# Kernel optimization log

Hardware: AMD Instinct MI355X
Metric: run time of the kernel (lower is better)

## Reference

```python
import jax, jax.numpy as jnp
import numpy as np

NUM_CATEGORIES = 32
INPUT_DIM = 1536
HIDDEN_DIM = 1024
OUTPUT_DIM = 1024
B, T = 128, 32


def setup_inputs() -> dict:
    key = jax.random.key(0)
    k_x, k_cat, k_w1, k_w2 = jax.random.split(key, 4)
    x = jax.random.normal(k_x, (B, T, INPUT_DIM), dtype=jnp.float32)
    cat_ids = jax.random.randint(k_cat, (B,), 0, NUM_CATEGORIES)
    # CategorySpecificLinear params: W ~ 0.02*randn, b = zeros
    W1 = 0.02 * jax.random.normal(k_w1, (NUM_CATEGORIES, INPUT_DIM, HIDDEN_DIM), dtype=jnp.float32)
    b1 = jnp.zeros((NUM_CATEGORIES, HIDDEN_DIM), dtype=jnp.float32)
    W2 = 0.02 * jax.random.normal(k_w2, (NUM_CATEGORIES, HIDDEN_DIM, OUTPUT_DIM), dtype=jnp.float32)
    b2 = jnp.zeros((NUM_CATEGORIES, OUTPUT_DIM), dtype=jnp.float32)
    return {"x": x, "cat_ids": cat_ids, "W1": W1, "b1": b1, "W2": W2, "b2": b2}


def _cat_linear(x, W, b, cat_ids):
    # x: (B, T, D_in); W: (C, D_in, D_out); b: (C, D_out)
    # torch: bmm(x, W[cat_ids]) + b[cat_ids].unsqueeze(1)
    return jnp.einsum("btd,bdh->bth", x, W[cat_ids]) + b[cat_ids][:, None, :]


def reference(x, cat_ids, W1, b1, W2, b2):
    # CategorySpecificMLP.forward
    hidden = jax.nn.relu(_cat_linear(x, W1, b1, cat_ids))  # (B, T, H)
    return _cat_linear(hidden, W2, b2, cat_ids)            # (B, T, O)
```

## Files before the change

kernel.cpp:

```cpp
#include <hip/hip_runtime.h>
#include <hip/hip_bf16.h>
#include <stdint.h>

#define NCAT 32
#define DIN  1536
#define DMID 1024
#define NB   128
#define TT   32

#define BM 128
#define BN 64
#define BK 32
#define LDA 40
#define MAXG 56

typedef __attribute__((ext_vector_type(8))) short short8;
typedef __attribute__((ext_vector_type(4))) float f32x4;

static __device__ __forceinline__ unsigned int pk2bf(float lo, float hi) {
  unsigned short a = __builtin_bit_cast(unsigned short, __float2bfloat16(lo));
  unsigned short b = __builtin_bit_cast(unsigned short, __float2bfloat16(hi));
  return ((unsigned int)b << 16) | (unsigned int)a;
}

static __device__ __forceinline__ void bar_noflush() {
  asm volatile("s_waitcnt lgkmcnt(0)" ::: "memory");
  __builtin_amdgcn_s_barrier();
  asm volatile("" ::: "memory");
}

__global__ void build_groups(const int* __restrict__ cat_ids, int* __restrict__ wsi) {
  __shared__ int cats[NB];
  __shared__ int cnt[NCAT];
  __shared__ int off[NCAT];
  int t = threadIdx.x;
  cats[t] = cat_ids[t];
  __syncthreads();
  if (t < NCAT) {
    int n = 0;
    for (int b = 0; b < NB; b++) n += (cats[b] == t);
    cnt[t] = n;
  }
  __syncthreads();
  if (t == 0) {
    int acc = 0;
    for (int c = 0; c < NCAT; c++) { off[c] = acc; acc += cnt[c]; }
  }
  __syncthreads();
  if (t < NCAT) {
    int o = off[t];
    for (int b = 0; b < NB; b++)
      if (cats[b] == t) wsi[o++] = b;
  }
  if (t == 0) {
    for (int s = 0; s < MAXG; s++) {
      wsi[132 + s * 4 + 0] = 0;
      wsi[132 + s * 4 + 1] = 0;
      wsi[132 + s * 4 + 2] = 0;
    }
    int rload[8];
    for (int r = 0; r < 8; r++) rload[r] = 0;
    for (int c = 0; c < NCAT; c++) {
      int n = cnt[c];
      if (n == 0) continue;
      int o = off[c];
      int r = 0;
      for (int k = 1; k < 8; k++) if (rload[k] < rload[r]) r = k;
      for (int j = 0; j < n; j += 4) {
        if (rload[r] >= 7) {
          r = 0;
          for (int k = 1; k < 8; k++) if (rload[k] < rload[r]) r = k;
        }
        int s = r + 8 * rload[r];
        rload[r]++;
        wsi[132 + s * 4 + 0] = c;
        wsi[132 + s * 4 + 1] = o + j;
        wsi[132 + s * 4 + 2] = (n - j) < 4 ? (n - j) : 4;
      }
    }
    wsi[128] = MAXG;
  }
}

template <int LAYER>
__global__ __launch_bounds__(256)
void mlp_gemm(const void* __restrict__ Ain, const float* __restrict__ W,
              const float* __restrict__ bias, const int* __restrict__ wsi,
              void* __restrict__ Out, int K) {
  const int l    = blockIdx.y * 16 + blockIdx.x;
  const int xcd  = l & 7;
  const int m    = l >> 3;
  const int slot = xcd + 8 * (m >> 4);
  const int cat   = wsi[132 + slot * 4 + 0];
  const int start = wsi[132 + slot * 4 + 1];
  const int cnt   = wsi[132 + slot * 4 + 2];
  if (cnt == 0) return;
  const int n0 = (m & 15) * BN;

  __shared__ unsigned short As[2][BM * LDA];
  __shared__ unsigned short Bs[2][4 * BN * 8];

  const int tid  = threadIdx.x;
  const int lane = tid & 63;
  const int w    = tid >> 6;

  const int arow  = tid >> 1;
  const int khalf = (tid & 1) * 16;
  const int lb    = arow >> 5;
  const int tok   = arow & 31;
  const int lbc   = lb < (cnt - 1) ? lb : (cnt - 1);
  const int batch = wsi[start + lbc];
  const long grow = (long)(batch * TT + tok);

  const float* Wcol = W + (size_t)cat * (size_t)K * 1024 + n0 + lane;

  f32x4 acc[4][2];
#pragma unroll
  for (int i = 0; i < 4; i++)
#pragma unroll
    for (int j = 0; j < 2; j++) acc[i][j] = (f32x4){0.f, 0.f, 0.f, 0.f};

  const int wm  = (w >> 1) * 64;
  const int wn  = (w & 1) * 32;
  const int kg  = lane >> 4;
  const int c16 = lane & 15;

  auto load_tile = [&](int k0, float4 ar[4], uint4 ah[2], float br[8]) {
    if constexpr (LAYER == 1) {
      const float* ap = (const float*)Ain + grow * (long)K + k0 + khalf;
      ar[0] = *(const float4*)(ap + 0);
      ar[1] = *(const float4*)(ap + 4);
      ar[2] = *(const float4*)(ap + 8);
      ar[3] = *(const float4*)(ap + 12);
    } else {
      const uint4* ap = (const uint4*)((const unsigned short*)Ain + grow * (long)K + k0 + khalf);
      ah[0] = ap[0];
      ah[1] = ap[1];
    }
    const float* bp = Wcol + (size_t)(k0 + w * 8) * 1024;
#pragma unroll
    for (int r = 0; r < 8; r++) br[r] = bp[(size_t)r * 1024];
  };

  auto store_tile = [&](int buf, const float4 ar[4], const uint4 ah[2], const float br[8]) {
    if constexpr (LAYER == 1) {
      uint4 aw0 = make_uint4(pk2bf(ar[0].x, ar[0].y), pk2bf(ar[0].z, ar[0].w),
                             pk2bf(ar[1].x, ar[1].y), pk2bf(ar[1].z, ar[1].w));
      uint4 aw1 = make_uint4(pk2bf(ar[2].x, ar[2].y), pk2bf(ar[2].z, ar[2].w),
                             pk2bf(ar[3].x, ar[3].y), pk2bf(ar[3].z, ar[3].w));
      *(uint4*)&As[buf][arow * LDA + khalf]     = aw0;
      *(uint4*)&As[buf][arow * LDA + khalf + 8] = aw1;
    } else {
      *(uint4*)&As[buf][arow * LDA + khalf]     = ah[0];
      *(uint4*)&As[buf][arow * LDA + khalf + 8] = ah[1];
    }
    uint4 bw = make_uint4(pk2bf(br[0], br[1]), pk2bf(br[2], br[3]),
                          pk2bf(br[4], br[5]), pk2bf(br[6], br[7]));
    *(uint4*)&Bs[buf][(w * BN + lane) * 8] = bw;
  };

  auto compute = [&](int buf) {
    short8 afrag[4], bfrag[2];
#pragma unroll
    for (int i = 0; i < 4; i++)
      afrag[i] = *(const short8*)&As[buf][(wm + i * 16 + c16) * LDA + kg * 8];
#pragma unroll
    for (int j = 0; j < 2; j++)
      bfrag[j] = *(const short8*)&Bs[buf][(kg * BN + wn + j * 16 + c16) * 8];
#pragma unroll
    for (int i = 0; i < 4; i++)
#pragma unroll
      for (int j = 0; j < 2; j++)
        acc[i][j] = __builtin_amdgcn_mfma_f32_16x16x32_bf16(afrag[i], bfrag[j], acc[i][j], 0, 0, 0);
  };

  float4 arA[4]; uint4 ahA[2]; float brA[8];
  float4 arB[4]; uint4 ahB[2]; float brB[8];

  const int nt = K / BK;

  load_tile(0, arA, ahA, brA);
  load_tile(BK, arB, ahB, brB);
  store_tile(0, arA, ahA, brA);
  bar_noflush();

  for (int t = 0; t + 2 <= nt; t += 2) {
    if (t + 2 < nt) load_tile((t + 2) * BK, arA, ahA, brA);
    store_tile(1, arB, ahB, brB);
    compute(0);
    bar_noflush();

    if (t + 3 < nt) load_tile((t + 3) * BK, arB, ahB, brB);
    if (t + 2 < nt) store_tile(0, arA, ahA, brA);
    compute(1);
    bar_noflush();
  }

  const int rquad = (lane >> 4) * 4;
#pragma unroll
  for (int i = 0; i < 4; i++) {
#pragma unroll
    for (int j = 0; j < 2; j++) {
      int gcol = n0 + wn + j * 16 + c16;
      float bb = bias[cat * 1024 + gcol];
#pragma unroll
      for (int r = 0; r < 4; r++) {
        int lrow = wm + i * 16 + rquad + r;
        int lb2 = lrow >> 5;
        if (lb2 < cnt) {
          int b2 = wsi[start + lb2];
          long orow = (long)(b2 * TT + (lrow & 31));
          float v = acc[i][j][r] + bb;
          if constexpr (LAYER == 1) {
            v = fmaxf(v, 0.f);
            ((unsigned short*)Out)[orow * DMID + gcol] =
                __builtin_bit_cast(unsigned short, __float2bfloat16(v));
          } else {
            ((float*)Out)[orow * 1024 + gcol] = v;
          }
        }
      }
    }
  }
}

extern "C" void kernel_launch(void* const* d_in, const int* in_sizes, int n_in,
                              void* d_out, int out_size, void* d_ws, size_t ws_size,
                              hipStream_t stream) {
  const float* x       = (const float*)d_in[0];
  const int*   cat_ids = (const int*)d_in[1];
  const float* W1      = (const float*)d_in[2];
  const float* b1      = (const float*)d_in[3];
  const float* W2      = (const float*)d_in[4];
  const float* b2      = (const float*)d_in[5];
  float* out = (float*)d_out;

  int* wsi = (int*)d_ws;
  unsigned short* hidden = (unsigned short*)((char*)d_ws + 8192);

  build_groups<<<dim3(1), dim3(128), 0, stream>>>(cat_ids, wsi);
  mlp_gemm<1><<<dim3(1024 / BN, MAXG), dim3(256), 0, stream>>>(
      (const void*)x, W1, b1, wsi, (void*)hidden, DIN);
  mlp_gemm<2><<<dim3(1024 / BN, MAXG), dim3(256), 0, stream>>>(
      (const void*)hidden, W2, b2, wsi, (void*)out, DMID);
}
```

Baseline: 486.3 us.

## Stream A tiles into LDS via direct global-to-LDS loads with swizzled layout

```diff
diff --git a/kernel.cpp b/kernel.cpp
--- a/kernel.cpp
+++ b/kernel.cpp
@@ -11,7 +11,6 @@
 #define BM 128
 #define BN 64
 #define BK 32
-#define LDA 40
 #define MAXG 56
 
 typedef __attribute__((ext_vector_type(8))) short short8;
@@ -23,10 +22,15 @@
   return ((unsigned int)b << 16) | (unsigned int)a;
 }
 
-static __device__ __forceinline__ void bar_noflush() {
-  asm volatile("s_waitcnt lgkmcnt(0)" ::: "memory");
-  __builtin_amdgcn_s_barrier();
-  asm volatile("" ::: "memory");
+static __device__ __forceinline__ unsigned int cvtpk(float lo, float hi) {
+  unsigned int r;
+  asm volatile("v_cvt_pk_bf16_f32 %0, %1, %2" : "=v"(r) : "v"(lo), "v"(hi));
+  return r;
+}
+
+static __device__ __forceinline__ void dma16(const void* g, void* l) {
+  __builtin_amdgcn_global_load_lds((const __attribute__((address_space(1))) void*)g,
+                                   (__attribute__((address_space(3))) void*)l, 16, 0, 0);
 }
 
 __global__ void build_groups(const int* __restrict__ cat_ids, int* __restrict__ wsi) {
@@ -97,73 +101,86 @@
   if (cnt == 0) return;
   const int n0 = (m & 15) * BN;
 
-  __shared__ unsigned short As[2][BM * LDA];
+  constexpr int ROWB   = (LAYER == 1) ? 128 : 64;
+  constexpr int ABYTES = BM * ROWB;
+  __shared__ __align__(16) unsigned char Asmem[2][ABYTES];
   __shared__ unsigned short Bs[2][4 * BN * 8];
 
   const int tid  = threadIdx.x;
   const int lane = tid & 63;
   const int w    = tid >> 6;
 
-  const int arow  = tid >> 1;
-  const int khalf = (tid & 1) * 16;
-  const int lb    = arow >> 5;
-  const int tok   = arow & 31;
-  const int lbc   = lb < (cnt - 1) ? lb : (cnt - 1);
-  const int batch = wsi[start + lbc];
-  const long grow = (long)(batch * TT + tok);
-
-  const float* Wcol = W + (size_t)cat * (size_t)K * 1024 + n0 + lane;
-
-  f32x4 acc[4][2];
-#pragma unroll
-  for (int i = 0; i < 4; i++)
-#pragma unroll
-    for (int j = 0; j < 2; j++) acc[i][j] = (f32x4){0.f, 0.f, 0.f, 0.f};
-
   const int wm  = (w >> 1) * 64;
   const int wn  = (w & 1) * 32;
   const int kg  = lane >> 4;
+  const int kg2 = kg << 1;
   const int c16 = lane & 15;
 
-  auto load_tile = [&](int k0, float4 ar[4], uint4 ah[2], float br[8]) {
+  const int batchW = wsi[start + (w < cnt ? w : cnt - 1)];
+  const float* alane1 = nullptr;
+  const unsigned short* alane2 = nullptr;
+  if constexpr (LAYER == 1) {
+    const int r8 = lane >> 3, c8 = lane & 7;
+    alane1 = (const float*)Ain + ((size_t)batchW * TT + r8) * K + ((c8 ^ r8) << 2);
+  } else {
+    const int r4 = lane >> 2, c4 = lane & 3;
+    alane2 = (const unsigned short*)Ain + ((size_t)batchW * TT + r4) * K + ((c4 ^ (r4 & 3)) << 3);
+  }
+
+  auto dmaA = [&](int tile, int buf) {
+    const int k0 = tile * BK;
     if constexpr (LAYER == 1) {
-      const float* ap = (const float*)Ain + grow * (long)K + k0 + khalf;
-      ar[0] = *(const float4*)(ap + 0);
-      ar[1] = *(const float4*)(ap + 4);
-      ar[2] = *(const float4*)(ap + 8);
-      ar[3] = *(const float4*)(ap + 12);
+#pragma unroll
+      for (int q = 0; q < 4; q++)
+        dma16(alane1 + (size_t)q * 8 * K + k0, &Asmem[buf][(w * 32 + q * 8) * 128]);
     } else {
-      const uint4* ap = (const uint4*)((const unsigned short*)Ain + grow * (long)K + k0 + khalf);
-      ah[0] = ap[0];
-      ah[1] = ap[1];
-    }
-    const float* bp = Wcol + (size_t)(k0 + w * 8) * 1024;
+#pragma unroll
+      for (int q = 0; q < 2; q++)
+        dma16(alane2 + (size_t)q * 16 * K + k0, &Asmem[buf][(w * 32 + q * 16) * 64]);
+    }
+  };
+
+  const float* Wcol = W + (size_t)cat * (size_t)K * 1024 + n0 + lane;
+  auto loadB = [&](int tile, float br[8]) {
+    const float* bp = Wcol + (size_t)(tile * BK + w * 8) * 1024;
 #pragma unroll
     for (int r = 0; r < 8; r++) br[r] = bp[(size_t)r * 1024];
   };
-
-  auto store_tile = [&](int buf, const float4 ar[4], const uint4 ah[2], const float br[8]) {
-    if constexpr (LAYER == 1) {
-      uint4 aw0 = make_uint4(pk2bf(ar[0].x, ar[0].y), pk2bf(ar[0].z, ar[0].w),
-                             pk2bf(ar[1].x, ar[1].y), pk2bf(ar[1].z, ar[1].w));
-      uint4 aw1 = make_uint4(pk2bf(ar[2].x, ar[2].y), pk2bf(ar[2].z, ar[2].w),
-                             pk2bf(ar[3].x, ar[3].y), pk2bf(ar[3].z, ar[3].w));
-      *(uint4*)&As[buf][arow * LDA + khalf]     = aw0;
-      *(uint4*)&As[buf][arow * LDA + khalf + 8] = aw1;
-    } else {
-      *(uint4*)&As[buf][arow * LDA + khalf]     = ah[0];
-      *(uint4*)&As[buf][arow * LDA + khalf + 8] = ah[1];
-    }
+  auto storeB = [&](int buf, const float br[8]) {
     uint4 bw = make_uint4(pk2bf(br[0], br[1]), pk2bf(br[2], br[3]),
                           pk2bf(br[4], br[5]), pk2bf(br[6], br[7]));
     *(uint4*)&Bs[buf][(w * BN + lane) * 8] = bw;
   };
 
+  f32x4 acc[4][2];
+#pragma unroll
+  for (int i = 0; i < 4; i++)
+#pragma unroll
+    for (int j = 0; j < 2; j++) acc[i][j] = (f32x4){0.f, 0.f, 0.f, 0.f};
+
   auto compute = [&](int buf) {
     short8 afrag[4], bfrag[2];
-#pragma unroll
-    for (int i = 0; i < 4; i++)
-      afrag[i] = *(const short8*)&As[buf][(wm + i * 16 + c16) * LDA + kg * 8];
+    if constexpr (LAYER == 1) {
+#pragma unroll
+      for (int i = 0; i < 4; i++) {
+        const int row = wm + i * 16 + c16;
+        const float* rp = (const float*)&Asmem[buf][row * 128];
+        const int sw = row & 7;
+        float4 lo = *(const float4*)(rp + (((kg2 + 0) ^ sw) << 2));
+        float4 hi = *(const float4*)(rp + (((kg2 + 1) ^ sw) << 2));
+        uint4 u;
+        u.x = cvtpk(lo.x, lo.y); u.y = cvtpk(lo.z, lo.w);
+        u.z = cvtpk(hi.x, hi.y); u.w = cvtpk(hi.z, hi.w);
+        afrag[i] = __builtin_bit_cast(short8, u);
+      }
+    } else {
+#pragma unroll
+      for (int i = 0; i < 4; i++) {
+        const int row = wm + i * 16 + c16;
+        const unsigned short* rp = (const unsigned short*)&Asmem[buf][row * 64];
+        afrag[i] = *(const short8*)(rp + ((kg ^ (row & 3)) << 3));
+      }
+    }
 #pragma unroll
     for (int j = 0; j < 2; j++)
       bfrag[j] = *(const short8*)&Bs[buf][(kg * BN + wn + j * 16 + c16) * 8];
@@ -174,26 +191,40 @@
         acc[i][j] = __builtin_amdgcn_mfma_f32_16x16x32_bf16(afrag[i], bfrag[j], acc[i][j], 0, 0, 0);
   };
 
-  float4 arA[4]; uint4 ahA[2]; float brA[8];
-  float4 arB[4]; uint4 ahB[2]; float brB[8];
-
+  float brA[8], brB[8];
   const int nt = K / BK;
 
-  load_tile(0, arA, ahA, brA);
-  load_tile(BK, arB, ahB, brB);
-  store_tile(0, arA, ahA, brA);
-  bar_noflush();
-
-  for (int t = 0; t + 2 <= nt; t += 2) {
-    if (t + 2 < nt) load_tile((t + 2) * BK, arA, ahA, brA);
-    store_tile(1, arB, ahB, brB);
-    compute(0);
-    bar_noflush();
-
-    if (t + 3 < nt) load_tile((t + 3) * BK, arB, ahB, brB);
-    if (t + 2 < nt) store_tile(0, arA, ahA, brA);
-    compute(1);
-    bar_noflush();
+  dmaA(0, 0);
+  __builtin_amdgcn_sched_barrier(0);
+  loadB(0, brA);
+  loadB(1 < nt ? 1 : 0, brB);
+  storeB(0, brA);
+  asm volatile("s_waitcnt lgkmcnt(0)" ::: "memory");
+  __builtin_amdgcn_s_barrier();
+
+  for (int t = 0; t < nt; t += 2) {
+    {
+      const int tn = (t + 1 < nt) ? t + 1 : nt - 1;
+      const int tb = (t + 2 < nt) ? t + 2 : nt - 1;
+      dmaA(tn, 1);
+      __builtin_amdgcn_sched_barrier(0);
+      loadB(tb, brA);
+      storeB(1, brB);
+      compute(0);
+      asm volatile("s_waitcnt vmcnt(8) lgkmcnt(0)" ::: "memory");
+      __builtin_amdgcn_s_barrier();
+    }
+    {
+      const int tn = (t + 2 < nt) ? t + 2 : nt - 1;
+      const int tb = (t + 3 < nt) ? t + 3 : nt - 1;
+      dmaA(tn, 0);
+      __builtin_amdgcn_sched_barrier(0);
+      loadB(tb, brB);
+      storeB(0, brA);
+      compute(1);
+      asm volatile("s_waitcnt vmcnt(8) lgkmcnt(0)" ::: "memory");
+      __builtin_amdgcn_s_barrier();
+    }
   }
 
   const int rquad = (lane >> 4) * 4;
```

Result: faster. 438.6 us (-9.8%).

## Deepen GEMM software pipeline to triple-buffered LDS with longer-latency B prefetch

Applied to the files above, without the earlier changes.

```diff
diff --git a/kernel.cpp b/kernel.cpp
--- a/kernel.cpp
+++ b/kernel.cpp
@@ -23,7 +23,7 @@
   return ((unsigned int)b << 16) | (unsigned int)a;
 }
 
-static __device__ __forceinline__ void bar_noflush() {
+static __device__ __forceinline__ void bar_lds() {
   asm volatile("s_waitcnt lgkmcnt(0)" ::: "memory");
   __builtin_amdgcn_s_barrier();
   asm volatile("" ::: "memory");
@@ -97,8 +97,8 @@
   if (cnt == 0) return;
   const int n0 = (m & 15) * BN;
 
-  __shared__ unsigned short As[2][BM * LDA];
-  __shared__ unsigned short Bs[2][4 * BN * 8];
+  __shared__ unsigned short Asm[3][BM * LDA];
+  __shared__ unsigned short Bsm[3][4 * BN * 8];
 
   const int tid  = threadIdx.x;
   const int lane = tid & 63;
@@ -125,7 +125,8 @@
   const int kg  = lane >> 4;
   const int c16 = lane & 15;
 
-  auto load_tile = [&](int k0, float4 ar[4], uint4 ah[2], float br[8]) {
+  auto loadA = [&](int tile, float4 ar[4], uint4 ah[2]) {
+    const int k0 = tile * BK;
     if constexpr (LAYER == 1) {
       const float* ap = (const float*)Ain + grow * (long)K + k0 + khalf;
       ar[0] = *(const float4*)(ap + 0);
@@ -137,36 +138,38 @@
       ah[0] = ap[0];
       ah[1] = ap[1];
     }
-    const float* bp = Wcol + (size_t)(k0 + w * 8) * 1024;
-#pragma unroll
-    for (int r = 0; r < 8; r++) br[r] = bp[(size_t)r * 1024];
-  };
-
-  auto store_tile = [&](int buf, const float4 ar[4], const uint4 ah[2], const float br[8]) {
+  };
+  auto storeA = [&](unsigned short* buf, const float4 ar[4], const uint4 ah[2]) {
     if constexpr (LAYER == 1) {
       uint4 aw0 = make_uint4(pk2bf(ar[0].x, ar[0].y), pk2bf(ar[0].z, ar[0].w),
                              pk2bf(ar[1].x, ar[1].y), pk2bf(ar[1].z, ar[1].w));
       uint4 aw1 = make_uint4(pk2bf(ar[2].x, ar[2].y), pk2bf(ar[2].z, ar[2].w),
                              pk2bf(ar[3].x, ar[3].y), pk2bf(ar[3].z, ar[3].w));
-      *(uint4*)&As[buf][arow * LDA + khalf]     = aw0;
-      *(uint4*)&As[buf][arow * LDA + khalf + 8] = aw1;
+      *(uint4*)&buf[arow * LDA + khalf]     = aw0;
+      *(uint4*)&buf[arow * LDA + khalf + 8] = aw1;
     } else {
-      *(uint4*)&As[buf][arow * LDA + khalf]     = ah[0];
-      *(uint4*)&As[buf][arow * LDA + khalf + 8] = ah[1];
-    }
+      *(uint4*)&buf[arow * LDA + khalf]     = ah[0];
+      *(uint4*)&buf[arow * LDA + khalf + 8] = ah[1];
+    }
+  };
+  auto loadB = [&](int tile, float br[8]) {
+    const float* bp = Wcol + (size_t)(tile * BK + w * 8) * 1024;
+#pragma unroll
+    for (int r = 0; r < 8; r++) br[r] = bp[(size_t)r * 1024];
+  };
+  auto storeB = [&](unsigned short* buf, const float br[8]) {
     uint4 bw = make_uint4(pk2bf(br[0], br[1]), pk2bf(br[2], br[3]),
                           pk2bf(br[4], br[5]), pk2bf(br[6], br[7]));
-    *(uint4*)&Bs[buf][(w * BN + lane) * 8] = bw;
-  };
-
-  auto compute = [&](int buf) {
+    *(uint4*)&buf[(w * BN + lane) * 8] = bw;
+  };
+  auto compute = [&](const unsigned short* Ab, const unsigned short* Bb) {
     short8 afrag[4], bfrag[2];
 #pragma unroll
     for (int i = 0; i < 4; i++)
-      afrag[i] = *(const short8*)&As[buf][(wm + i * 16 + c16) * LDA + kg * 8];
+      afrag[i] = *(const short8*)&Ab[(wm + i * 16 + c16) * LDA + kg * 8];
 #pragma unroll
     for (int j = 0; j < 2; j++)
-      bfrag[j] = *(const short8*)&Bs[buf][(kg * BN + wn + j * 16 + c16) * 8];
+      bfrag[j] = *(const short8*)&Bb[(kg * BN + wn + j * 16 + c16) * 8];
 #pragma unroll
     for (int i = 0; i < 4; i++)
 #pragma unroll
@@ -174,27 +177,44 @@
         acc[i][j] = __builtin_amdgcn_mfma_f32_16x16x32_bf16(afrag[i], bfrag[j], acc[i][j], 0, 0, 0);
   };
 
-  float4 arA[4]; uint4 ahA[2]; float brA[8];
-  float4 arB[4]; uint4 ahB[2]; float brB[8];
+  unsigned short *A0 = Asm[0], *A1 = Asm[1], *A2 = Asm[2];
+  unsigned short *B0 = Bsm[0], *B1 = Bsm[1], *B2 = Bsm[2];
+
+  float4 ar0[4], ar1[4]; uint4 ah0[2], ah1[2];
+  float br0[8], br1[8], br2[8], br3[8];
 
   const int nt = K / BK;
 
-  load_tile(0, arA, ahA, brA);
-  load_tile(BK, arB, ahB, brB);
-  store_tile(0, arA, ahA, brA);
-  bar_noflush();
-
-  for (int t = 0; t + 2 <= nt; t += 2) {
-    if (t + 2 < nt) load_tile((t + 2) * BK, arA, ahA, brA);
-    store_tile(1, arB, ahB, brB);
-    compute(0);
-    bar_noflush();
-
-    if (t + 3 < nt) load_tile((t + 3) * BK, arB, ahB, brB);
-    if (t + 2 < nt) store_tile(0, arA, ahA, brA);
-    compute(1);
-    bar_noflush();
-  }
+  loadA(0, ar0, ah0);
+  loadA(1, ar1, ah1);
+  loadB(0, br0); loadB(1, br1); loadB(2, br2); loadB(3, br3);
+  storeA(A0, ar0, ah0); storeB(B0, br0);
+  loadA(2, ar0, ah0);
+  storeA(A1, ar1, ah1); storeB(B1, br1);
+  bar_lds();
+
+#define STEP(TT_, ARL, AHL, BRL, ARS, AHS, BRS)                     \
+  {                                                                 \
+    const int t_ = (TT_);                                           \
+    const int tl3 = (t_ + 3 < nt) ? t_ + 3 : nt - 1;                \
+    const int tl4 = (t_ + 4 < nt) ? t_ + 4 : nt - 1;                \
+    loadA(tl3, ARL, AHL);                                           \
+    loadB(tl4, BRL);                                                \
+    storeA(A2, ARS, AHS);                                           \
+    storeB(B2, BRS);                                                \
+    compute(A0, B0);                                                \
+    bar_lds();                                                      \
+    unsigned short* tA = A0; A0 = A1; A1 = A2; A2 = tA;             \
+    unsigned short* tB = B0; B0 = B1; B1 = B2; B2 = tB;             \
+  }
+
+  for (int t = 0; t < nt; t += 4) {
+    STEP(t + 0, ar1, ah1, br0, ar0, ah0, br2)
+    STEP(t + 1, ar0, ah0, br1, ar1, ah1, br3)
+    STEP(t + 2, ar1, ah1, br2, ar0, ah0, br0)
+    STEP(t + 3, ar0, ah0, br3, ar1, ah1, br1)
+  }
+#undef STEP
 
   const int rquad = (lane >> 4) * 4;
 #pragma unroll
```

Measured after the change: 495.0 us. About the same (+1.8%).
